# Kernel optimization log

Hardware: AMD Instinct MI355X
Metric: run time of the kernel (lower is better)

Reference implementation:

```python
import jax, jax.numpy as jnp
import numpy as np

B, S, E = 16, 1024, 512
D = 2 * E            # dim of concatenated embeddings, input to QKV and MLP
H1, H2 = 2048, 1024  # hidden_dims
SCALE = float(1.0 / np.sqrt(E))  # code scales by embedding_dim**0.5 (the init arg, not D)


def setup_inputs() -> dict:
    key = jax.random.key(0)
    k = jax.random.split(key, 12)

    def lin_w(kk, fan_in, fan_out):
        return jax.random.normal(kk, (fan_in, fan_out), jnp.float32) * float(1.0 / np.sqrt(fan_in))

    return {
        "emb1": jax.random.normal(k[0], (B, S, E), jnp.float32),
        "emb2": jax.random.normal(k[1], (B, S, E), jnp.float32),
        # query-row masks; all ones (a 0 would -inf an entire softmax row -> NaN)
        "mask1": jnp.ones((B, S // 2), jnp.int32),
        "mask2": jnp.ones((B, S // 2), jnp.int32),
        "Wq": lin_w(k[2], D, D), "bq": jnp.zeros((D,), jnp.float32),
        "Wk": lin_w(k[3], D, D), "bk": jnp.zeros((D,), jnp.float32),
        "Wv": lin_w(k[4], D, D), "bv": jnp.zeros((D,), jnp.float32),
        "W1": lin_w(k[5], D, H1), "b1": jnp.zeros((H1,), jnp.float32),
        "W2": lin_w(k[6], H1, H2), "b2": jnp.zeros((H2,), jnp.float32),
        "W3": lin_w(k[7], H2, 1), "b3": jnp.zeros((1,), jnp.float32),
    }


def reference(emb1, emb2, mask1, mask2, Wq, bq, Wk, bk, Wv, bv, W1, b1, W2, b2, W3, b3):
    x = jnp.concatenate([emb1, emb2], axis=-1)        # [B, S, D]
    mask = jnp.concatenate([mask1, mask2], axis=-1)   # [B, S] (query-row mask)

    # QKV self-attention with query-only mask
    Q = x @ Wq + bq
    K = x @ Wk + bk
    V = x @ Wv + bv
    scores = jnp.einsum("bqd,bkd->bqk", Q, K) * SCALE  # [B, S, S]
    scores = jnp.where(mask[:, :, None] == 0, -jnp.inf, scores)
    attn = jax.nn.softmax(scores, axis=-1)
    attended = jnp.einsum("bqk,bkd->bqd", attn, V)     # [B, S, D]

    # MLP head (Dropout is identity in eval mode)
    h = jax.nn.relu(attended @ W1 + b1)
    h = jax.nn.relu(h @ W2 + b2)
    logits = h @ W3 + b3                               # [B, S, 1]
    return jax.nn.sigmoid(logits)
```

## Files before the change

kernel.cpp:

```cpp
#include <hip/hip_runtime.h>
#include <math.h>

#define DEV __device__ __forceinline__
#define SB0() __builtin_amdgcn_sched_barrier(0)

typedef unsigned short u16;
typedef unsigned int   u32;
typedef __bf16 bf16x8 __attribute__((ext_vector_type(8)));
typedef float  f32x4  __attribute__((ext_vector_type(4)));
typedef u16    u16x8  __attribute__((ext_vector_type(8)));
typedef u16    u16x4  __attribute__((ext_vector_type(4)));

DEV u16 f2b(float f) {
  u32 u = __builtin_bit_cast(u32, f);
  u = (u + 0x7FFFu + ((u >> 16) & 1u)) >> 16;
  return (u16)u;
}
DEV float b2f(u16 h) { u32 u = (u32)h << 16; return __builtin_bit_cast(float, u); }

DEV void gl_lds16(const u16* g, u16* l) {
  __builtin_amdgcn_global_load_lds((const __attribute__((address_space(1))) void*)g,
                                   (__attribute__((address_space(3))) void*)l, 16, 0, 0);
}

__global__ __launch_bounds__(256) void prep(
    const float* __restrict__ e1, const float* __restrict__ e2, u16* __restrict__ xb,
    const float* __restrict__ Wq, const float* __restrict__ Wk, const float* __restrict__ Wv,
    const float* __restrict__ W1, const float* __restrict__ W2,
    u16* __restrict__ WTQKV, u16* __restrict__ W1T, u16* __restrict__ W2T,
    const float* __restrict__ bq, const float* __restrict__ bk, float* __restrict__ bf) {
  __shared__ float tile[64][65];
  const int bid = blockIdx.x;
  if (bid < 8192) {
    const size_t idx = ((size_t)bid * 256 + threadIdx.x) * 8;
    const int d = (int)(idx & 1023);
    const size_t row = idx >> 10;
    const float* s = (d < 512) ? (e1 + row * 512 + d) : (e2 + row * 512 + (d - 512));
    f32x4 a = *(const f32x4*)s;
    f32x4 b = *(const f32x4*)(s + 4);
    u16x8 o;
    o[0]=f2b(a[0]); o[1]=f2b(a[1]); o[2]=f2b(a[2]); o[3]=f2b(a[3]);
    o[4]=f2b(b[0]); o[5]=f2b(b[1]); o[6]=f2b(b[2]); o[7]=f2b(b[3]);
    *(u16x8*)(xb + idx) = o;
    return;
  }
  if (bid >= 9984) {
    int i = (bid - 9984) * 256 + threadIdx.x;
    bf[i] = (i < 1024) ? bq[i] : bk[i - 1024];
    return;
  }
  const float* W; u16* WT; int ldi, ldo, bx, by;
  if (bid < 8448)      { W = Wq; WT = WTQKV;              ldi = 1024; ldo = 1024; int v = bid - 8192; bx = v & 15; by = v >> 4; }
  else if (bid < 8704) { W = Wk; WT = WTQKV + 1024*1024;  ldi = 1024; ldo = 1024; int v = bid - 8448; bx = v & 15; by = v >> 4; }
  else if (bid < 8960) { W = Wv; WT = WTQKV + 2048*1024;  ldi = 1024; ldo = 1024; int v = bid - 8704; bx = v & 15; by = v >> 4; }
  else if (bid < 9472) { W = W1; WT = W1T;                ldi = 2048; ldo = 1024; int v = bid - 8960; bx = v & 31; by = v >> 5; }
  else                 { W = W2; WT = W2T;                ldi = 1024; ldo = 2048; int v = bid - 9472; bx = v & 15; by = v >> 4; }
  const int tx = threadIdx.x & 63, ty = threadIdx.x >> 6;
  const int r0 = by * 64, c0 = bx * 64;
#pragma unroll
  for (int i = 0; i < 16; ++i)
    tile[ty + 4*i][tx] = W[(size_t)(r0 + ty + 4*i) * ldi + c0 + tx];
  __syncthreads();
#pragma unroll
  for (int i = 0; i < 16; ++i)
    WT[(size_t)(c0 + ty + 4*i) * ldo + r0 + tx] = f2b(tile[tx][ty + 4*i]);
}

template<int MODE>
__global__ __launch_bounds__(512, 2) void gemm256(
    const u16* __restrict__ A, int lda, long long sA,
    const u16* __restrict__ B, int ldb, long long sB,
    void* __restrict__ C, int ldc, long long sC,
    const float* __restrict__ bias, float scale, int K,
    const int* __restrict__ mk1, const int* __restrict__ mk2,
    float* __restrict__ rsw, const float* __restrict__ w3, float* __restrict__ lg) {
  __shared__ __align__(16) u16 lds[2][2][16384];

  const int t  = threadIdx.x;
  const int ln = t & 63, wv = t >> 6;

  int bx, by, bz;
  {
    const int gx = gridDim.x, gy = gridDim.y, gz = gridDim.z;
    const int nwg = gx * gy * gz;
    const int F = (blockIdx.z * gy + blockIdx.y) * gx + blockIdx.x;
    const int q = nwg >> 3;
    const int L = (F & 7) * q + (F >> 3);
    if (gz > 1) {
      const int pb = gx * gy;
      bz = L / pb; const int r = L - bz * pb;
      by = r / gx; bx = r - by * gx;
    } else {
      bz = 0;
      const int sh = ((gy & 7) == 0) ? 8 : 4;
      const int sw = gx * sh;
      const int sy = L / sw; const int r = L - sy * sw;
      bx = r / sh; by = sy * sh + (r - bx * sh);
    }
  }
  const int m0 = by * 256, n0 = bx * 256;
  A += (size_t)bz * (size_t)sA; B += (size_t)bz * (size_t)sB;

  const int gl = (ln & 7) ^ (ln >> 3);
  const u16* gAs = A + (size_t)(m0 + (t >> 3)) * lda + gl * 8;
  const u16* gBs = B + (size_t)(n0 + (t >> 3)) * ldb + gl * 8;

  const int l15 = ln & 15, lhi = ln >> 4;
  const int wm = (wv >> 2) * 128, wn = (wv & 3) * 64;
  const int colk0 = ((lhi ^ (l15 & 7)) << 3);
  const int colk1 = (((4 + lhi) ^ (l15 & 7)) << 3);
  const int rcA = (wv >> 2) * 8192 + l15 * 64;
  const int rcB = ((wv & 3) >> 1) * 8192 + (wv & 1) * 4096 + l15 * 64;

  f32x4 acc[8][4] = {};
  bf16x8 Af[4][2], Bf[4][2];
  const int KT = K >> 6, NIT = KT >> 1;

#define STG(T, OP, H, LD, GS)                                              \
  if ((T) < KT) {                                                          \
    const u16* _s = (GS) + (size_t)(H) * 128 * (size_t)(LD) + (size_t)(T) * 64; \
    u16* _d = &lds[(T) & 1][OP][(H) * 8192 + wv * 512];                    \
    gl_lds16(_s, _d); gl_lds16(_s + 64 * (size_t)(LD), _d + 4096);         \
  }
#define RDA(BUF, ILO) {                                                    \
  _Pragma("unroll") for (int ii = 0; ii < 4; ++ii) {                       \
    Af[ii][0] = *(const bf16x8*)&lds[BUF][0][rcA + ((ILO) + ii) * 1024 + colk0]; \
    Af[ii][1] = *(const bf16x8*)&lds[BUF][0][rcA + ((ILO) + ii) * 1024 + colk1]; } }
#define RDB(BUF, JLO) {                                                    \
  _Pragma("unroll") for (int jj = 0; jj < 2; ++jj) {                       \
    Bf[(JLO) + jj][0] = *(const bf16x8*)&lds[BUF][1][rcB + ((JLO) + jj) * 1024 + colk0]; \
    Bf[(JLO) + jj][1] = *(const bf16x8*)&lds[BUF][1][rcB + ((JLO) + jj) * 1024 + colk1]; } }
#define MM(ILO, JLO) {                                                     \
  _Pragma("unroll") for (int ii = 0; ii < 4; ++ii)                         \
  _Pragma("unroll") for (int jj = 0; jj < 2; ++jj) {                       \
    acc[(ILO)+ii][(JLO)+jj] = __builtin_amdgcn_mfma_f32_16x16x32_bf16(Af[ii][0], Bf[(JLO)+jj][0], acc[(ILO)+ii][(JLO)+jj], 0, 0, 0); \
    acc[(ILO)+ii][(JLO)+jj] = __builtin_amdgcn_mfma_f32_16x16x32_bf16(Af[ii][1], Bf[(JLO)+jj][1], acc[(ILO)+ii][(JLO)+jj], 0, 0, 0); } }
#define BAR() __builtin_amdgcn_s_barrier()
#define PRIO(x) __builtin_amdgcn_s_setprio(x)

  STG(0, 0, 0, lda, gAs); STG(0, 0, 1, lda, gAs);
  STG(0, 1, 0, ldb, gBs); STG(0, 1, 1, ldb, gBs);
  STG(1, 1, 0, ldb, gBs); STG(1, 1, 1, ldb, gBs);
  asm volatile("s_waitcnt vmcnt(4)" ::: "memory");
  SB0(); BAR();

  for (int it = 0; it < NIT; ++it) {
    const int T0 = it << 1, T1 = T0 + 1;
    RDB(0, 0); RDA(0, 0); STG(T1, 0, 0, lda, gAs);
    BAR();
    PRIO(1); MM(0, 0); PRIO(0); BAR();
    RDB(0, 2); STG(T1, 0, 1, lda, gAs);
    BAR();
    PRIO(1); MM(0, 2); PRIO(0); BAR();
    RDA(0, 4); STG(T0 + 2, 1, 0, ldb, gBs);
    BAR();
    PRIO(1); MM(4, 0); PRIO(0); BAR();
    STG(T0 + 2, 1, 1, ldb, gBs);
    BAR();
    PRIO(1); MM(4, 2); PRIO(0);
    if (T0 + 2 < KT) { asm volatile("s_waitcnt vmcnt(4)" ::: "memory"); }
    else             { asm volatile("s_waitcnt vmcnt(0)" ::: "memory"); }
    SB0(); BAR();
    RDB(1, 0); RDA(1, 0); STG(T0 + 2, 0, 0, lda, gAs);
    BAR();
    PRIO(1); MM(0, 0); PRIO(0); BAR();
    RDB(1, 2); STG(T0 + 2, 0, 1, lda, gAs);
    BAR();
    PRIO(1); MM(0, 2); PRIO(0); BAR();
    RDA(1, 4); STG(T0 + 3, 1, 0, ldb, gBs);
    BAR();
    PRIO(1); MM(4, 0); PRIO(0); BAR();
    STG(T0 + 3, 1, 1, ldb, gBs);
    BAR();
    PRIO(1); MM(4, 2); PRIO(0);
    if (T0 + 3 < KT) { asm volatile("s_waitcnt vmcnt(4)" ::: "memory"); }
    SB0(); BAR();
  }
#undef STG
#undef RDA
#undef RDB
#undef MM
#undef BAR
#undef PRIO

  const size_t cb = (size_t)bz * (size_t)sC;

  if (MODE == 5) {
    float w3v[4];
#pragma unroll
    for (int j = 0; j < 4; ++j) w3v[j] = w3[n0 + wn + j * 16 + l15];
#pragma unroll
    for (int i = 0; i < 8; ++i) {
      const int rg = m0 + wm + i * 16 + lhi * 4;
#pragma unroll
      for (int r = 0; r < 4; ++r) {
        float s = 0.f;
#pragma unroll
        for (int j = 0; j < 4; ++j) {
          float v = acc[i][j][r] + bias[n0 + wn + j * 16 + l15];
          v = fmaxf(v, 0.f);
          s += v * w3v[j];
        }
        s += __shfl_xor(s, 1, 64); s += __shfl_xor(s, 2, 64);
        s += __shfl_xor(s, 4, 64); s += __shfl_xor(s, 8, 64);
        if (l15 == 0) atomicAdd(&lg[rg + r], s);
      }
    }
    return;
  }

  u16* ep = ((u16*)lds) + wv * 8192;

  if (MODE == 3) {
#pragma unroll
    for (int i = 0; i < 8; ++i) {
#pragma unroll
      for (int r = 0; r < 4; ++r) {
        const int rr = m0 + wm + i * 16 + lhi * 4 + r;
        const int mk = (rr < 512) ? mk1[bz * 512 + rr] : mk2[bz * 512 + rr - 512];
        const int lrow = i * 16 + lhi * 4 + r;
        float s = 0.f;
#pragma unroll
        for (int j = 0; j < 4; ++j) {
          float e = (mk != 0) ? __expf(acc[i][j][r] * scale) : 0.f;
          const u16 eb = f2b(e);
          s += b2f(eb);
          const int lcol = (j * 16 + l15) ^ (((lrow >> 2) & 7) << 3);
          ep[lrow * 64 + lcol] = eb;
        }
        s += __shfl_xor(s, 1, 64); s += __shfl_xor(s, 2, 64);
        s += __shfl_xor(s, 4, 64); s += __shfl_xor(s, 8, 64);
        if (l15 == 0) atomicAdd(&rsw[(size_t)bz * 1024 + rr], s);
      }
    }
  } else {
#pragma unroll
    for (int i = 0; i < 8; ++i) {
      const int rl = wm + i * 16 + lhi * 4;
      float rv[4];
#pragma unroll
      for (int r = 0; r < 4; ++r) {
        if (MODE == 2)      rv[r] = bias[m0 + rl + r];
        else if (MODE == 4) rv[r] = 1.f / rsw[(size_t)bz * 1024 + m0 + rl + r];
        else                rv[r] = 0.f;
      }
#pragma unroll
      for (int j = 0; j < 4; ++j) {
        const float cbv = (MODE == 0 || MODE == 1) ? bias[n0 + wn + j * 16 + l15] : 0.f;
#pragma unroll
        for (int r = 0; r < 4; ++r) {
          float v;
          if (MODE == 4)      v = acc[i][j][r] * rv[r];
          else if (MODE == 2) v = acc[i][j][r] + rv[r];
          else                v = acc[i][j][r] + cbv;
          if (MODE == 1) v = fmaxf(v, 0.f);
          const int lrow = i * 16 + lhi * 4 + r;
          const int lcol = (j * 16 + l15) ^ (((lrow >> 2) & 7) << 3);
          ep[lrow * 64 + lcol] = f2b(v);
        }
      }
    }
  }
  asm volatile("s_waitcnt lgkmcnt(0)" ::: "memory");
  SB0();
  const int l3 = ln >> 3, c0 = (ln & 7) * 8;
#pragma unroll
  for (int rep = 0; rep < 16; ++rep) {
    const int lr = rep * 8 + l3;
    const int cs = c0 ^ (((lr >> 2) & 7) << 3);
    u16x8 v = *(const u16x8*)&ep[lr * 64 + cs];
    *(u16x8*)((u16*)C + cb + (size_t)(m0 + wm + lr) * ldc + n0 + wn + c0) = v;
  }
}

__global__ __launch_bounds__(256) void sigmoid_k(
    const float* __restrict__ lg, const float* __restrict__ b3, float* __restrict__ out) {
  const int i = blockIdx.x * 256 + threadIdx.x;
  out[i] = 1.f / (1.f + __expf(-(lg[i] + b3[0])));
}

extern "C" void kernel_launch(void* const* d_in, const int* in_sizes, int n_in,
                              void* d_out, int out_size, void* d_ws, size_t ws_size,
                              hipStream_t stream) {
  (void)in_sizes; (void)n_in; (void)out_size; (void)ws_size;
  const float* emb1 = (const float*)d_in[0];
  const float* emb2 = (const float*)d_in[1];
  const int*   mask1 = (const int*)d_in[2];
  const int*   mask2 = (const int*)d_in[3];
  const float* Wq = (const float*)d_in[4];  const float* bq = (const float*)d_in[5];
  const float* Wk = (const float*)d_in[6];  const float* bk = (const float*)d_in[7];
  const float* Wv = (const float*)d_in[8];  const float* bv = (const float*)d_in[9];
  const float* W1 = (const float*)d_in[10]; const float* b1 = (const float*)d_in[11];
  const float* W2 = (const float*)d_in[12]; const float* b2 = (const float*)d_in[13];
  const float* W3 = (const float*)d_in[14]; const float* b3 = (const float*)d_in[15];

  char* ws = (char*)d_ws;
  u16*  XB    = (u16*)(ws + 0);
  u16*  QK    = (u16*)(ws + 33554432);
  u16*  VT    = (u16*)(ws + 100663296);
  u16*  ATT   = (u16*)(ws + 134217728);
  u16*  WTQKV = (u16*)(ws + 167772160);
  u16*  W1T   = (u16*)(ws + 174063616);
  u16*  W2T   = (u16*)(ws + 178257920);
  float* BF_  = (float*)(ws + 182452224);
  float* RS   = (float*)(ws + 182460416);
  float* LG   = (float*)(ws + 182525952);
  u16*  E     = XB;
  u16*  H1    = QK;
  float* out  = (float*)d_out;

  const float SCALE = 0.04419417382415922f;

  hipMemsetAsync(RS, 0, 131072, stream);

  prep<<<9992, 256, 0, stream>>>(emb1, emb2, XB, Wq, Wk, Wv, W1, W2,
                                 WTQKV, W1T, W2T, bq, bk, BF_);

  gemm256<0><<<dim3(8, 64, 1), 512, 0, stream>>>(
      XB, 1024, 0, WTQKV, 1024, 0, QK, 2048, 0, BF_, 1.f, 1024,
      nullptr, nullptr, nullptr, nullptr, nullptr);
  gemm256<2><<<dim3(64, 4, 1), 512, 0, stream>>>(
      WTQKV + 2048 * 1024, 1024, 0, XB, 1024, 0, VT, 16384, 0, bv, 1.f, 1024,
      nullptr, nullptr, nullptr, nullptr, nullptr);
  gemm256<3><<<dim3(4, 4, 16), 512, 0, stream>>>(
      QK, 2048, 2097152LL, QK + 1024, 2048, 2097152LL,
      E, 1024, 1048576LL, nullptr, SCALE, 1024,
      mask1, mask2, RS, nullptr, nullptr);
  gemm256<4><<<dim3(4, 4, 16), 512, 0, stream>>>(
      E, 1024, 1048576LL, VT, 16384, 1024LL,
      ATT, 1024, 1048576LL, nullptr, 1.f, 1024,
      nullptr, nullptr, RS, nullptr, nullptr);
  gemm256<1><<<dim3(8, 64, 1), 512, 0, stream>>>(
      ATT, 1024, 0, W1T, 1024, 0, H1, 2048, 0, b1, 1.f, 1024,
      nullptr, nullptr, nullptr, nullptr, nullptr);
  gemm256<5><<<dim3(4, 64, 1), 512, 0, stream>>>(
      H1, 2048, 0, W2T, 2048, 0, nullptr, 1024, 0, b2, 1.f, 2048,
      nullptr, nullptr, nullptr, W3, LG);
  sigmoid_k<<<64, 256, 0, stream>>>(LG, b3, out);
}
```

Before: 348.6 us.

## Shrink GEMM tile to 128x256 with BK=32 simple double-buffered loop

Replaces the 256x256, BK=64 GEMM with its hand-scheduled split-phase pipeline by a 128x256 tile using BK=32 K-steps and a simple double-buffered loop. Each step issues one A and two B global-to-LDS loads, reads 4+4 fragments and runs 16 MFMAs per wave. Smaller LDS use and fewer accumulators allow launch bounds of 4 blocks per SM, and grid sizes double to match. The goal is more occupancy and latency hiding, at the cost of half the reuse per tile, more LDS traffic per FLOP, and a full vmcnt(0) wait plus barrier every K-step.

```diff
diff --git a/kernel.cpp b/kernel.cpp
--- a/kernel.cpp
+++ b/kernel.cpp
@@ -9,7 +9,6 @@
 typedef __bf16 bf16x8 __attribute__((ext_vector_type(8)));
 typedef float  f32x4  __attribute__((ext_vector_type(4)));
 typedef u16    u16x8  __attribute__((ext_vector_type(8)));
-typedef u16    u16x4  __attribute__((ext_vector_type(4)));
 
 DEV u16 f2b(float f) {
   u32 u = __builtin_bit_cast(u32, f);
@@ -67,14 +66,14 @@
 }
 
 template<int MODE>
-__global__ __launch_bounds__(512, 2) void gemm256(
+__global__ __launch_bounds__(512, 4) void gemm256(
     const u16* __restrict__ A, int lda, long long sA,
     const u16* __restrict__ B, int ldb, long long sB,
     void* __restrict__ C, int ldc, long long sC,
     const float* __restrict__ bias, float scale, int K,
     const int* __restrict__ mk1, const int* __restrict__ mk2,
     float* __restrict__ rsw, const float* __restrict__ w3, float* __restrict__ lg) {
-  __shared__ __align__(16) u16 lds[2][2][16384];
+  __shared__ __align__(16) u16 lds[32768];
 
   const int t  = threadIdx.x;
   const int ln = t & 63, wv = t >> 6;
@@ -92,96 +91,79 @@
       by = r / gx; bx = r - by * gx;
     } else {
       bz = 0;
-      const int sh = ((gy & 7) == 0) ? 8 : 4;
-      const int sw = gx * sh;
+      const int sw = gx * 8;
       const int sy = L / sw; const int r = L - sy * sw;
-      bx = r / sh; by = sy * sh + (r - bx * sh);
+      bx = r >> 3; by = sy * 8 + (r & 7);
     }
   }
-  const int m0 = by * 256, n0 = bx * 256;
+  const int m0 = by * 128, n0 = bx * 256;
   A += (size_t)bz * (size_t)sA; B += (size_t)bz * (size_t)sB;
 
-  const int gl = (ln & 7) ^ (ln >> 3);
-  const u16* gAs = A + (size_t)(m0 + (t >> 3)) * lda + gl * 8;
-  const u16* gBs = B + (size_t)(n0 + (t >> 3)) * ldb + gl * 8;
+  const int srow = t >> 2;
+  const int sg   = (t & 3) ^ ((t >> 3) & 3);
+  const u16* gA = A + (size_t)(m0 + srow) * lda + sg * 8;
+  const u16* gB = B + (size_t)(n0 + srow) * ldb + sg * 8;
+  const size_t b128r = (size_t)128 * ldb;
+  const int ldst = wv * 512;
 
   const int l15 = ln & 15, lhi = ln >> 4;
-  const int wm = (wv >> 2) * 128, wn = (wv & 3) * 64;
-  const int colk0 = ((lhi ^ (l15 & 7)) << 3);
-  const int colk1 = (((4 + lhi) ^ (l15 & 7)) << 3);
-  const int rcA = (wv >> 2) * 8192 + l15 * 64;
-  const int rcB = ((wv & 3) >> 1) * 8192 + (wv & 1) * 4096 + l15 * 64;
-
-  f32x4 acc[8][4] = {};
-  bf16x8 Af[4][2], Bf[4][2];
-  const int KT = K >> 6, NIT = KT >> 1;
-
-#define STG(T, OP, H, LD, GS)                                              \
-  if ((T) < KT) {                                                          \
-    const u16* _s = (GS) + (size_t)(H) * 128 * (size_t)(LD) + (size_t)(T) * 64; \
-    u16* _d = &lds[(T) & 1][OP][(H) * 8192 + wv * 512];                    \
-    gl_lds16(_s, _d); gl_lds16(_s + 64 * (size_t)(LD), _d + 4096);         \
-  }
-#define RDA(BUF, ILO) {                                                    \
-  _Pragma("unroll") for (int ii = 0; ii < 4; ++ii) {                       \
-    Af[ii][0] = *(const bf16x8*)&lds[BUF][0][rcA + ((ILO) + ii) * 1024 + colk0]; \
-    Af[ii][1] = *(const bf16x8*)&lds[BUF][0][rcA + ((ILO) + ii) * 1024 + colk1]; } }
-#define RDB(BUF, JLO) {                                                    \
-  _Pragma("unroll") for (int jj = 0; jj < 2; ++jj) {                       \
-    Bf[(JLO) + jj][0] = *(const bf16x8*)&lds[BUF][1][rcB + ((JLO) + jj) * 1024 + colk0]; \
-    Bf[(JLO) + jj][1] = *(const bf16x8*)&lds[BUF][1][rcB + ((JLO) + jj) * 1024 + colk1]; } }
-#define MM(ILO, JLO) {                                                     \
-  _Pragma("unroll") for (int ii = 0; ii < 4; ++ii)                         \
-  _Pragma("unroll") for (int jj = 0; jj < 2; ++jj) {                       \
-    acc[(ILO)+ii][(JLO)+jj] = __builtin_amdgcn_mfma_f32_16x16x32_bf16(Af[ii][0], Bf[(JLO)+jj][0], acc[(ILO)+ii][(JLO)+jj], 0, 0, 0); \
-    acc[(ILO)+ii][(JLO)+jj] = __builtin_amdgcn_mfma_f32_16x16x32_bf16(Af[ii][1], Bf[(JLO)+jj][1], acc[(ILO)+ii][(JLO)+jj], 0, 0, 0); } }
-#define BAR() __builtin_amdgcn_s_barrier()
-#define PRIO(x) __builtin_amdgcn_s_setprio(x)
-
-  STG(0, 0, 0, lda, gAs); STG(0, 0, 1, lda, gAs);
-  STG(0, 1, 0, ldb, gBs); STG(0, 1, 1, ldb, gBs);
-  STG(1, 1, 0, ldb, gBs); STG(1, 1, 1, ldb, gBs);
-  asm volatile("s_waitcnt vmcnt(4)" ::: "memory");
-  SB0(); BAR();
-
-  for (int it = 0; it < NIT; ++it) {
-    const int T0 = it << 1, T1 = T0 + 1;
-    RDB(0, 0); RDA(0, 0); STG(T1, 0, 0, lda, gAs);
-    BAR();
-    PRIO(1); MM(0, 0); PRIO(0); BAR();
-    RDB(0, 2); STG(T1, 0, 1, lda, gAs);
-    BAR();
-    PRIO(1); MM(0, 2); PRIO(0); BAR();
-    RDA(0, 4); STG(T0 + 2, 1, 0, ldb, gBs);
-    BAR();
-    PRIO(1); MM(4, 0); PRIO(0); BAR();
-    STG(T0 + 2, 1, 1, ldb, gBs);
-    BAR();
-    PRIO(1); MM(4, 2); PRIO(0);
-    if (T0 + 2 < KT) { asm volatile("s_waitcnt vmcnt(4)" ::: "memory"); }
-    else             { asm volatile("s_waitcnt vmcnt(0)" ::: "memory"); }
-    SB0(); BAR();
-    RDB(1, 0); RDA(1, 0); STG(T0 + 2, 0, 0, lda, gAs);
-    BAR();
-    PRIO(1); MM(0, 0); PRIO(0); BAR();
-    RDB(1, 2); STG(T0 + 2, 0, 1, lda, gAs);
-    BAR();
-    PRIO(1); MM(0, 2); PRIO(0); BAR();
-    RDA(1, 4); STG(T0 + 3, 1, 0, ldb, gBs);
-    BAR();
-    PRIO(1); MM(4, 0); PRIO(0); BAR();
-    STG(T0 + 3, 1, 1, ldb, gBs);
-    BAR();
-    PRIO(1); MM(4, 2); PRIO(0);
-    if (T0 + 3 < KT) { asm volatile("s_waitcnt vmcnt(4)" ::: "memory"); }
-    SB0(); BAR();
-  }
-#undef STG
-#undef RDA
-#undef RDB
-#undef MM
-#undef BAR
-#undef PRIO
+  const int wm = (wv >> 2) * 64, wn = (wv & 3) * 64;
+
+  int offA[4], offB[4];
+#pragma unroll
+  for (int i = 0; i < 4; ++i) {
+    const int r = wm + i * 16 + l15;
+    offA[i] = r * 32 + ((lhi ^ ((r >> 1) & 3)) << 3);
+  }
+#pragma unroll
+  for (int j = 0; j < 4; ++j) {
+    const int r = wn + j * 16 + l15;
+    offB[j] = 4096 + r * 32 + ((lhi ^ ((r >> 1) & 3)) << 3);
+  }
+
+  f32x4 acc[4][4] = {};
+  const int KT = K >> 5;
+
+#define STAGE(T)                                                          \
+  {                                                                       \
+    const int rb = (T) & 1;                                               \
+    const u16* _a = gA + (size_t)(T) * 32;                                \
+    const u16* _b = gB + (size_t)(T) * 32;                                \
+    gl_lds16(_a, &lds[rb * 12288 + ldst]);                                \
+    gl_lds16(_b, &lds[rb * 12288 + 4096 + ldst]);                         \
+    gl_lds16(_b + b128r, &lds[rb * 12288 + 8192 + ldst]);                 \
+  }
+#define MF(i, j, Av, Bv) \
+  acc[i][j] = __builtin_amdgcn_mfma_f32_16x16x32_bf16(Av, Bv, acc[i][j], 0, 0, 0)
+
+  STAGE(0);
+  asm volatile("s_waitcnt vmcnt(0)" ::: "memory");
+  SB0();
+  __builtin_amdgcn_s_barrier();
+
+  for (int kt = 0; kt < KT; ++kt) {
+    if (kt + 1 < KT) STAGE(kt + 1);
+    const u16* bb = &lds[(kt & 1) * 12288];
+    bf16x8 a0 = *(const bf16x8*)&bb[offA[0]];
+    bf16x8 a1 = *(const bf16x8*)&bb[offA[1]];
+    bf16x8 a2 = *(const bf16x8*)&bb[offA[2]];
+    bf16x8 a3 = *(const bf16x8*)&bb[offA[3]];
+    bf16x8 b0 = *(const bf16x8*)&bb[offB[0]];
+    bf16x8 b1 = *(const bf16x8*)&bb[offB[1]];
+    bf16x8 b2 = *(const bf16x8*)&bb[offB[2]];
+    bf16x8 b3 = *(const bf16x8*)&bb[offB[3]];
+    __builtin_amdgcn_s_setprio(1);
+    MF(0,0,a0,b0); MF(0,1,a0,b1); MF(0,2,a0,b2); MF(0,3,a0,b3);
+    MF(1,0,a1,b0); MF(1,1,a1,b1); MF(1,2,a1,b2); MF(1,3,a1,b3);
+    MF(2,0,a2,b0); MF(2,1,a2,b1); MF(2,2,a2,b2); MF(2,3,a2,b3);
+    MF(3,0,a3,b0); MF(3,1,a3,b1); MF(3,2,a3,b2); MF(3,3,a3,b3);
+    __builtin_amdgcn_s_setprio(0);
+    asm volatile("s_waitcnt vmcnt(0)" ::: "memory");
+    SB0();
+    __builtin_amdgcn_s_barrier();
+  }
+#undef STAGE
+#undef MF
 
   const size_t cb = (size_t)bz * (size_t)sC;
 
@@ -190,7 +172,7 @@
 #pragma unroll
     for (int j = 0; j < 4; ++j) w3v[j] = w3[n0 + wn + j * 16 + l15];
 #pragma unroll
-    for (int i = 0; i < 8; ++i) {
+    for (int i = 0; i < 4; ++i) {
       const int rg = m0 + wm + i * 16 + lhi * 4;
 #pragma unroll
       for (int r = 0; r < 4; ++r) {
@@ -209,11 +191,11 @@
     return;
   }
 
-  u16* ep = ((u16*)lds) + wv * 8192;
+  u16* ep = lds + wv * 4096;
 
   if (MODE == 3) {
 #pragma unroll
-    for (int i = 0; i < 8; ++i) {
+    for (int i = 0; i < 4; ++i) {
 #pragma unroll
       for (int r = 0; r < 4; ++r) {
         const int rr = m0 + wm + i * 16 + lhi * 4 + r;
@@ -235,7 +217,7 @@
     }
   } else {
 #pragma unroll
-    for (int i = 0; i < 8; ++i) {
+    for (int i = 0; i < 4; ++i) {
       const int rl = wm + i * 16 + lhi * 4;
       float rv[4];
 #pragma unroll
@@ -265,7 +247,7 @@
   SB0();
   const int l3 = ln >> 3, c0 = (ln & 7) * 8;
 #pragma unroll
-  for (int rep = 0; rep < 16; ++rep) {
+  for (int rep = 0; rep < 8; ++rep) {
     const int lr = rep * 8 + l3;
     const int cs = c0 ^ (((lr >> 2) & 7) << 3);
     u16x8 v = *(const u16x8*)&ep[lr * 64 + cs];
@@ -316,24 +298,24 @@
   prep<<<9992, 256, 0, stream>>>(emb1, emb2, XB, Wq, Wk, Wv, W1, W2,
                                  WTQKV, W1T, W2T, bq, bk, BF_);
 
-  gemm256<0><<<dim3(8, 64, 1), 512, 0, stream>>>(
+  gemm256<0><<<dim3(8, 128, 1), 512, 0, stream>>>(
       XB, 1024, 0, WTQKV, 1024, 0, QK, 2048, 0, BF_, 1.f, 1024,
       nullptr, nullptr, nullptr, nullptr, nullptr);
-  gemm256<2><<<dim3(64, 4, 1), 512, 0, stream>>>(
+  gemm256<2><<<dim3(64, 8, 1), 512, 0, stream>>>(
       WTQKV + 2048 * 1024, 1024, 0, XB, 1024, 0, VT, 16384, 0, bv, 1.f, 1024,
       nullptr, nullptr, nullptr, nullptr, nullptr);
-  gemm256<3><<<dim3(4, 4, 16), 512, 0, stream>>>(
+  gemm256<3><<<dim3(4, 8, 16), 512, 0, stream>>>(
       QK, 2048, 2097152LL, QK + 1024, 2048, 2097152LL,
       E, 1024, 1048576LL, nullptr, SCALE, 1024,
       mask1, mask2, RS, nullptr, nullptr);
-  gemm256<4><<<dim3(4, 4, 16), 512, 0, stream>>>(
+  gemm256<4><<<dim3(4, 8, 16), 512, 0, stream>>>(
       E, 1024, 1048576LL, VT, 16384, 1024LL,
       ATT, 1024, 1048576LL, nullptr, 1.f, 1024,
       nullptr, nullptr, RS, nullptr, nullptr);
-  gemm256<1><<<dim3(8, 64, 1), 512, 0, stream>>>(
+  gemm256<1><<<dim3(8, 128, 1), 512, 0, stream>>>(
       ATT, 1024, 0, W1T, 1024, 0, H1, 2048, 0, b1, 1.f, 1024,
       nullptr, nullptr, nullptr, nullptr, nullptr);
-  gemm256<5><<<dim3(4, 64, 1), 512, 0, stream>>>(
+  gemm256<5><<<dim3(4, 128, 1), 512, 0, stream>>>(
       H1, 2048, 0, W2T, 2048, 0, nullptr, 1024, 0, b2, 1.f, 2048,
       nullptr, nullptr, nullptr, W3, LG);
   sigmoid_k<<<64, 256, 0, stream>>>(LG, b3, out);
```

Result: slower. 357.5 us (+2.5%).

## Fold Q and K projections into a single Wq·Wkᵀ product with rank-1 bias terms

Applied to the files above, without the earlier changes.

Instead of computing Q and K separately, precomputes M = Wq Wkᵀ in bf16 and a per-row x·M product, then forms scores as (xM)xᵀ. The bias terms become per-row and per-column vectors added in the softmax epilogue. This roughly halves the projection GEMM work. In exchange it adds small extra kernels and changes rounding because M is quantized to bf16.

```diff
diff --git a/kernel.cpp b/kernel.cpp
--- a/kernel.cpp
+++ b/kernel.cpp
@@ -9,7 +9,6 @@
 typedef __bf16 bf16x8 __attribute__((ext_vector_type(8)));
 typedef float  f32x4  __attribute__((ext_vector_type(4)));
 typedef u16    u16x8  __attribute__((ext_vector_type(8)));
-typedef u16    u16x4  __attribute__((ext_vector_type(4)));
 
 DEV u16 f2b(float f) {
   u32 u = __builtin_bit_cast(u32, f);
@@ -27,8 +26,8 @@
     const float* __restrict__ e1, const float* __restrict__ e2, u16* __restrict__ xb,
     const float* __restrict__ Wq, const float* __restrict__ Wk, const float* __restrict__ Wv,
     const float* __restrict__ W1, const float* __restrict__ W2,
-    u16* __restrict__ WTQKV, u16* __restrict__ W1T, u16* __restrict__ W2T,
-    const float* __restrict__ bq, const float* __restrict__ bk, float* __restrict__ bf) {
+    u16* __restrict__ Wqb, u16* __restrict__ Wkb,
+    u16* __restrict__ WvT, u16* __restrict__ W1T, u16* __restrict__ W2T) {
   __shared__ float tile[64][65];
   const int bid = blockIdx.x;
   if (bid < 8192) {
@@ -44,17 +43,23 @@
     *(u16x8*)(xb + idx) = o;
     return;
   }
-  if (bid >= 9984) {
-    int i = (bid - 9984) * 256 + threadIdx.x;
-    bf[i] = (i < 1024) ? bq[i] : bk[i - 1024];
+  if (bid < 9216) {
+    const int base = (bid < 8704) ? 8192 : 8704;
+    const float* src = (bid < 8704) ? Wq : Wk;
+    u16* dst = (bid < 8704) ? Wqb : Wkb;
+    const int off = ((bid - base) * 256 + threadIdx.x) * 8;
+    f32x4 a = *(const f32x4*)(src + off);
+    f32x4 b = *(const f32x4*)(src + off + 4);
+    u16x8 o;
+    o[0]=f2b(a[0]); o[1]=f2b(a[1]); o[2]=f2b(a[2]); o[3]=f2b(a[3]);
+    o[4]=f2b(b[0]); o[5]=f2b(b[1]); o[6]=f2b(b[2]); o[7]=f2b(b[3]);
+    *(u16x8*)(dst + off) = o;
     return;
   }
   const float* W; u16* WT; int ldi, ldo, bx, by;
-  if (bid < 8448)      { W = Wq; WT = WTQKV;              ldi = 1024; ldo = 1024; int v = bid - 8192; bx = v & 15; by = v >> 4; }
-  else if (bid < 8704) { W = Wk; WT = WTQKV + 1024*1024;  ldi = 1024; ldo = 1024; int v = bid - 8448; bx = v & 15; by = v >> 4; }
-  else if (bid < 8960) { W = Wv; WT = WTQKV + 2048*1024;  ldi = 1024; ldo = 1024; int v = bid - 8704; bx = v & 15; by = v >> 4; }
-  else if (bid < 9472) { W = W1; WT = W1T;                ldi = 2048; ldo = 1024; int v = bid - 8960; bx = v & 31; by = v >> 5; }
-  else                 { W = W2; WT = W2T;                ldi = 1024; ldo = 2048; int v = bid - 9472; bx = v & 15; by = v >> 4; }
+  if (bid < 9472)      { W = Wv; WT = WvT; ldi = 1024; ldo = 1024; int v = bid - 9216; bx = v & 15; by = v >> 4; }
+  else if (bid < 9984) { W = W1; WT = W1T; ldi = 2048; ldo = 1024; int v = bid - 9472; bx = v & 31; by = v >> 5; }
+  else                 { W = W2; WT = W2T; ldi = 1024; ldo = 2048; int v = bid - 9984; bx = v & 15; by = v >> 4; }
   const int tx = threadIdx.x & 63, ty = threadIdx.x >> 6;
   const int r0 = by * 64, c0 = bx * 64;
 #pragma unroll
@@ -64,6 +69,62 @@
 #pragma unroll
   for (int i = 0; i < 16; ++i)
     WT[(size_t)(c0 + ty + 4*i) * ldo + r0 + tx] = f2b(tile[tx][ty + 4*i]);
+}
+
+__global__ __launch_bounds__(256) void bias_vecs(
+    const float* __restrict__ Wq, const float* __restrict__ Wk,
+    const float* __restrict__ bq, const float* __restrict__ bk,
+    float* __restrict__ vq, float* __restrict__ vk, float* __restrict__ cc) {
+  const int bid = blockIdx.x;
+  if (bid == 512) {
+    __shared__ float red[256];
+    float s = 0.f;
+    for (int i = threadIdx.x; i < 1024; i += 256) s += bq[i] * bk[i];
+    red[threadIdx.x] = s; __syncthreads();
+    for (int o = 128; o > 0; o >>= 1) {
+      if ((int)threadIdx.x < o) red[threadIdx.x] += red[threadIdx.x + o];
+      __syncthreads();
+    }
+    if (threadIdx.x == 0) cc[0] = red[0];
+    return;
+  }
+  const float* W = (bid < 256) ? Wq : Wk;
+  const float* b = (bid < 256) ? bk : bq;
+  float* v = (bid < 256) ? vq : vk;
+  const int row = ((bid & 255) << 2) + (threadIdx.x >> 6);
+  const int ln = threadIdx.x & 63;
+  const float* p = W + (size_t)row * 1024 + ln * 16;
+  float s = 0.f;
+#pragma unroll
+  for (int m = 0; m < 16; ++m) s += p[m] * b[ln * 16 + m];
+#pragma unroll
+  for (int o = 32; o > 0; o >>= 1) s += __shfl_xor(s, o, 64);
+  if (ln == 0) v[row] = s;
+}
+
+__global__ __launch_bounds__(256) void uw_vecs(
+    const u16* __restrict__ xb, const float* __restrict__ vq,
+    const float* __restrict__ vk, const float* __restrict__ cc,
+    float* __restrict__ U, float* __restrict__ W_) {
+  const int row = blockIdx.x * 4 + (threadIdx.x >> 6);
+  const int ln = threadIdx.x & 63;
+  const u16* p = xb + (size_t)row * 1024 + ln * 16;
+  u16x8 x0 = *(const u16x8*)p;
+  u16x8 x1 = *(const u16x8*)(p + 8);
+  float dq = 0.f, dk = 0.f;
+#pragma unroll
+  for (int m = 0; m < 8; ++m) {
+    float xv = b2f(x0[m]);
+    dq += xv * vq[ln * 16 + m]; dk += xv * vk[ln * 16 + m];
+  }
+#pragma unroll
+  for (int m = 0; m < 8; ++m) {
+    float xv = b2f(x1[m]);
+    dq += xv * vq[ln * 16 + 8 + m]; dk += xv * vk[ln * 16 + 8 + m];
+  }
+#pragma unroll
+  for (int o = 32; o > 0; o >>= 1) { dq += __shfl_xor(dq, o, 64); dk += __shfl_xor(dk, o, 64); }
+  if (ln == 0) { U[row] = dq + cc[0]; W_[row] = dk; }
 }
 
 template<int MODE>
@@ -73,7 +134,9 @@
     void* __restrict__ C, int ldc, long long sC,
     const float* __restrict__ bias, float scale, int K,
     const int* __restrict__ mk1, const int* __restrict__ mk2,
-    float* __restrict__ rsw, const float* __restrict__ w3, float* __restrict__ lg) {
+    float* __restrict__ rsw, const float* __restrict__ uvec,
+    const float* __restrict__ wvec, const float* __restrict__ w3,
+    float* __restrict__ lg) {
   __shared__ __align__(16) u16 lds[2][2][16384];
 
   const int t  = threadIdx.x;
@@ -212,17 +275,22 @@
   u16* ep = ((u16*)lds) + wv * 8192;
 
   if (MODE == 3) {
+    float wv4[4];
+#pragma unroll
+    for (int j = 0; j < 4; ++j)
+      wv4[j] = wvec[(size_t)bz * 1024 + n0 + wn + j * 16 + l15];
 #pragma unroll
     for (int i = 0; i < 8; ++i) {
 #pragma unroll
       for (int r = 0; r < 4; ++r) {
         const int rr = m0 + wm + i * 16 + lhi * 4 + r;
         const int mk = (rr < 512) ? mk1[bz * 512 + rr] : mk2[bz * 512 + rr - 512];
+        const float uq = uvec[(size_t)bz * 1024 + rr];
         const int lrow = i * 16 + lhi * 4 + r;
         float s = 0.f;
 #pragma unroll
         for (int j = 0; j < 4; ++j) {
-          float e = (mk != 0) ? __expf(acc[i][j][r] * scale) : 0.f;
+          float e = (mk != 0) ? __expf((acc[i][j][r] + uq + wv4[j]) * scale) : 0.f;
           const u16 eb = f2b(e);
           s += b2f(eb);
           const int lcol = (j * 16 + l15) ^ (((lrow >> 2) & 7) << 3);
@@ -246,7 +314,7 @@
       }
 #pragma unroll
       for (int j = 0; j < 4; ++j) {
-        const float cbv = (MODE == 0 || MODE == 1) ? bias[n0 + wn + j * 16 + l15] : 0.f;
+        const float cbv = ((MODE == 0 || MODE == 1) && bias) ? bias[n0 + wn + j * 16 + l15] : 0.f;
 #pragma unroll
         for (int r = 0; r < 4; ++r) {
           float v;
@@ -296,45 +364,57 @@
 
   char* ws = (char*)d_ws;
   u16*  XB    = (u16*)(ws + 0);
-  u16*  QK    = (u16*)(ws + 33554432);
-  u16*  VT    = (u16*)(ws + 100663296);
+  u16*  XM    = (u16*)(ws + 33554432);
+  u16*  VT    = (u16*)(ws + 67108864);
+  u16*  E     = (u16*)(ws + 100663296);
   u16*  ATT   = (u16*)(ws + 134217728);
-  u16*  WTQKV = (u16*)(ws + 167772160);
-  u16*  W1T   = (u16*)(ws + 174063616);
-  u16*  W2T   = (u16*)(ws + 178257920);
-  float* BF_  = (float*)(ws + 182452224);
-  float* RS   = (float*)(ws + 182460416);
-  float* LG   = (float*)(ws + 182525952);
-  u16*  E     = XB;
-  u16*  H1    = QK;
+  u16*  WvT   = (u16*)(ws + 167772160);
+  u16*  Wqb   = (u16*)(ws + 169869312);
+  u16*  Wkb   = (u16*)(ws + 171966464);
+  u16*  MTb   = (u16*)(ws + 174063616);
+  u16*  W1T   = (u16*)(ws + 176160768);
+  u16*  W2T   = (u16*)(ws + 180355072);
+  float* VQ   = (float*)(ws + 184549376);
+  float* VK   = (float*)(ws + 184553472);
+  float* CC   = (float*)(ws + 184557568);
+  float* U    = (float*)(ws + 184561664);
+  float* W_   = (float*)(ws + 184627200);
+  float* RS   = (float*)(ws + 184692736);
+  float* LG   = (float*)(ws + 184758272);
+  u16*  H1    = XB;
   float* out  = (float*)d_out;
 
   const float SCALE = 0.04419417382415922f;
 
   hipMemsetAsync(RS, 0, 131072, stream);
 
-  prep<<<9992, 256, 0, stream>>>(emb1, emb2, XB, Wq, Wk, Wv, W1, W2,
-                                 WTQKV, W1T, W2T, bq, bk, BF_);
-
-  gemm256<0><<<dim3(8, 64, 1), 512, 0, stream>>>(
-      XB, 1024, 0, WTQKV, 1024, 0, QK, 2048, 0, BF_, 1.f, 1024,
-      nullptr, nullptr, nullptr, nullptr, nullptr);
+  prep<<<10496, 256, 0, stream>>>(emb1, emb2, XB, Wq, Wk, Wv, W1, W2,
+                                  Wqb, Wkb, WvT, W1T, W2T);
+  bias_vecs<<<513, 256, 0, stream>>>(Wq, Wk, bq, bk, VQ, VK, CC);
+  uw_vecs<<<4096, 256, 0, stream>>>(XB, VQ, VK, CC, U, W_);
+
+  gemm256<0><<<dim3(4, 4, 1), 512, 0, stream>>>(
+      Wkb, 1024, 0, Wqb, 1024, 0, MTb, 1024, 0, nullptr, 1.f, 1024,
+      nullptr, nullptr, nullptr, nullptr, nullptr, nullptr, nullptr);
+  gemm256<0><<<dim3(4, 64, 1), 512, 0, stream>>>(
+      XB, 1024, 0, MTb, 1024, 0, XM, 1024, 0, nullptr, 1.f, 1024,
+      nullptr, nullptr, nullptr, nullptr, nullptr, nullptr, nullptr);
   gemm256<2><<<dim3(64, 4, 1), 512, 0, stream>>>(
-      WTQKV + 2048 * 1024, 1024, 0, XB, 1024, 0, VT, 16384, 0, bv, 1.f, 1024,
-      nullptr, nullptr, nullptr, nullptr, nullptr);
+      WvT, 1024, 0, XB, 1024, 0, VT, 16384, 0, bv, 1.f, 1024,
+      nullptr, nullptr, nullptr, nullptr, nullptr, nullptr, nullptr);
   gemm256<3><<<dim3(4, 4, 16), 512, 0, stream>>>(
-      QK, 2048, 2097152LL, QK + 1024, 2048, 2097152LL,
+      XM, 1024, 1048576LL, XB, 1024, 1048576LL,
       E, 1024, 1048576LL, nullptr, SCALE, 1024,
-      mask1, mask2, RS, nullptr, nullptr);
+      mask1, mask2, RS, U, W_, nullptr, nullptr);
   gemm256<4><<<dim3(4, 4, 16), 512, 0, stream>>>(
       E, 1024, 1048576LL, VT, 16384, 1024LL,
       ATT, 1024, 1048576LL, nullptr, 1.f, 1024,
-      nullptr, nullptr, RS, nullptr, nullptr);
+      nullptr, nullptr, RS, nullptr, nullptr, nullptr, nullptr);
   gemm256<1><<<dim3(8, 64, 1), 512, 0, stream>>>(
       ATT, 1024, 0, W1T, 1024, 0, H1, 2048, 0, b1, 1.f, 1024,
-      nullptr, nullptr, nullptr, nullptr, nullptr);
+      nullptr, nullptr, nullptr, nullptr, nullptr, nullptr, nullptr);
   gemm256<5><<<dim3(4, 64, 1), 512, 0, stream>>>(
       H1, 2048, 0, W2T, 2048, 0, nullptr, 1024, 0, b2, 1.f, 2048,
-      nullptr, nullptr, nullptr, W3, LG);
+      nullptr, nullptr, nullptr, nullptr, nullptr, W3, LG);
   sigmoid_k<<<64, 256, 0, stream>>>(LG, b3, out);
 }
```

Result: slower. 368.0 us (+5.6%).

## Add 128x256-tile GEMM kernel with triple-buffered LDS for QK and W1 projections

Applied to the files above, without the earlier changes.

Introduces a new gemm128 kernel that uses 128x256 output tiles, a 3-stage LDS ring filled by direct global-to-LDS loads, and launch bounds allowing four workgroups per CU. It is used for the QK projection and the first MLP layer, doubling the grid to 1024 workgroups. The aim is better CU occupancy, more latency hiding and better load balance across the MI355X's compute units. In exchange each tile reuses its operands less, so global and LDS traffic per FLOP rises.

```diff
diff --git a/kernel.cpp b/kernel.cpp
--- a/kernel.cpp
+++ b/kernel.cpp
@@ -9,7 +9,6 @@
 typedef __bf16 bf16x8 __attribute__((ext_vector_type(8)));
 typedef float  f32x4  __attribute__((ext_vector_type(4)));
 typedef u16    u16x8  __attribute__((ext_vector_type(8)));
-typedef u16    u16x4  __attribute__((ext_vector_type(4)));
 
 DEV u16 f2b(float f) {
   u32 u = __builtin_bit_cast(u32, f);
@@ -273,6 +272,129 @@
   }
 }
 
+template<int MODE>
+__global__ __launch_bounds__(512, 4) void gemm128(
+    const u16* __restrict__ A, int lda,
+    const u16* __restrict__ B, int ldb,
+    void* __restrict__ C, int ldc,
+    const float* __restrict__ bias, int K) {
+  __shared__ __align__(16) u16 lds[3 * 12288];
+
+  const int t  = threadIdx.x;
+  const int ln = t & 63, wv = t >> 6;
+
+  int bx, by;
+  {
+    const int gx = gridDim.x, gy = gridDim.y;
+    const int nwg = gx * gy;
+    const int F = blockIdx.y * gx + blockIdx.x;
+    const int q = nwg >> 3;
+    const int L = (F & 7) * q + (F >> 3);
+    const int sw = gx * 8;
+    const int sy = L / sw; const int r = L - sy * sw;
+    bx = r >> 3; by = sy * 8 + (r & 7);
+  }
+  const int m0 = by * 128, n0 = bx * 256;
+
+  const int srow = t >> 2;
+  const int sg   = (t & 3) ^ ((t >> 3) & 3);
+  const u16* gA = A + (size_t)(m0 + srow) * lda + sg * 8;
+  const u16* gB = B + (size_t)(n0 + srow) * ldb + sg * 8;
+  const size_t b128r = (size_t)128 * ldb;
+  const int ldst = wv * 512;
+
+  const int l15 = ln & 15, lhi = ln >> 4;
+  const int wm = (wv >> 2) * 64, wn = (wv & 3) * 64;
+
+  int offA[4], offB[4];
+#pragma unroll
+  for (int i = 0; i < 4; ++i) {
+    const int r = wm + i * 16 + l15;
+    offA[i] = r * 32 + ((lhi ^ ((r >> 1) & 3)) << 3);
+  }
+#pragma unroll
+  for (int j = 0; j < 4; ++j) {
+    const int r = wn + j * 16 + l15;
+    offB[j] = 4096 + r * 32 + ((lhi ^ ((r >> 1) & 3)) << 3);
+  }
+
+  f32x4 acc[4][4] = {};
+  const int KT = K >> 5;
+
+#define STAGE(T, RB)                                                      \
+  {                                                                       \
+    const u16* _a = gA + (size_t)(T) * 32;                                \
+    const u16* _b = gB + (size_t)(T) * 32;                                \
+    gl_lds16(_a, &lds[(RB) * 12288 + ldst]);                              \
+    gl_lds16(_b, &lds[(RB) * 12288 + 4096 + ldst]);                       \
+    gl_lds16(_b + b128r, &lds[(RB) * 12288 + 8192 + ldst]);               \
+  }
+#define MF(i, j, Av, Bv) \
+  acc[i][j] = __builtin_amdgcn_mfma_f32_16x16x32_bf16(Av, Bv, acc[i][j], 0, 0, 0)
+
+  STAGE(0, 0); STAGE(1, 1);
+  asm volatile("s_waitcnt vmcnt(3)" ::: "memory");
+  SB0();
+  __builtin_amdgcn_s_barrier();
+
+  int rb_read = 0, rb_stage = 2;
+  for (int kt = 0; kt < KT; ++kt) {
+    if (kt + 2 < KT) STAGE(kt + 2, rb_stage);
+    const u16* bb = &lds[rb_read * 12288];
+    bf16x8 a0 = *(const bf16x8*)&bb[offA[0]];
+    bf16x8 a1 = *(const bf16x8*)&bb[offA[1]];
+    bf16x8 a2 = *(const bf16x8*)&bb[offA[2]];
+    bf16x8 a3 = *(const bf16x8*)&bb[offA[3]];
+    bf16x8 b0 = *(const bf16x8*)&bb[offB[0]];
+    bf16x8 b1 = *(const bf16x8*)&bb[offB[1]];
+    bf16x8 b2 = *(const bf16x8*)&bb[offB[2]];
+    bf16x8 b3 = *(const bf16x8*)&bb[offB[3]];
+    __builtin_amdgcn_s_setprio(1);
+    MF(0,0,a0,b0); MF(0,1,a0,b1); MF(0,2,a0,b2); MF(0,3,a0,b3);
+    MF(1,0,a1,b0); MF(1,1,a1,b1); MF(1,2,a1,b2); MF(1,3,a1,b3);
+    MF(2,0,a2,b0); MF(2,1,a2,b1); MF(2,2,a2,b2); MF(2,3,a2,b3);
+    MF(3,0,a3,b0); MF(3,1,a3,b1); MF(3,2,a3,b2); MF(3,3,a3,b3);
+    __builtin_amdgcn_s_setprio(0);
+    if (kt < KT - 2)       { asm volatile("s_waitcnt vmcnt(3)" ::: "memory"); }
+    else if (kt == KT - 2) { asm volatile("s_waitcnt vmcnt(0)" ::: "memory"); }
+    if (kt < KT - 1) {
+      SB0();
+      __builtin_amdgcn_s_barrier();
+    }
+    rb_read  = (rb_read  == 2) ? 0 : rb_read + 1;
+    rb_stage = (rb_stage == 2) ? 0 : rb_stage + 1;
+  }
+#undef STAGE
+#undef MF
+
+  u16* ep = lds + wv * 4096;
+#pragma unroll
+  for (int i = 0; i < 4; ++i) {
+#pragma unroll
+    for (int j = 0; j < 4; ++j) {
+      const float cbv = bias[n0 + wn + j * 16 + l15];
+#pragma unroll
+      for (int r = 0; r < 4; ++r) {
+        float v = acc[i][j][r] + cbv;
+        if (MODE == 1) v = fmaxf(v, 0.f);
+        const int lrow = i * 16 + lhi * 4 + r;
+        const int lcol = (j * 16 + l15) ^ (((lrow >> 2) & 7) << 3);
+        ep[lrow * 64 + lcol] = f2b(v);
+      }
+    }
+  }
+  asm volatile("s_waitcnt lgkmcnt(0)" ::: "memory");
+  SB0();
+  const int l3 = ln >> 3, c0 = (ln & 7) * 8;
+#pragma unroll
+  for (int rep = 0; rep < 8; ++rep) {
+    const int lr = rep * 8 + l3;
+    const int cs = c0 ^ (((lr >> 2) & 7) << 3);
+    u16x8 v = *(const u16x8*)&ep[lr * 64 + cs];
+    *(u16x8*)((u16*)C + (size_t)(m0 + wm + lr) * ldc + n0 + wn + c0) = v;
+  }
+}
+
 __global__ __launch_bounds__(256) void sigmoid_k(
     const float* __restrict__ lg, const float* __restrict__ b3, float* __restrict__ out) {
   const int i = blockIdx.x * 256 + threadIdx.x;
@@ -316,9 +438,8 @@
   prep<<<9992, 256, 0, stream>>>(emb1, emb2, XB, Wq, Wk, Wv, W1, W2,
                                  WTQKV, W1T, W2T, bq, bk, BF_);
 
-  gemm256<0><<<dim3(8, 64, 1), 512, 0, stream>>>(
-      XB, 1024, 0, WTQKV, 1024, 0, QK, 2048, 0, BF_, 1.f, 1024,
-      nullptr, nullptr, nullptr, nullptr, nullptr);
+  gemm128<0><<<dim3(8, 128, 1), 512, 0, stream>>>(
+      XB, 1024, WTQKV, 1024, QK, 2048, BF_, 1024);
   gemm256<2><<<dim3(64, 4, 1), 512, 0, stream>>>(
       WTQKV + 2048 * 1024, 1024, 0, XB, 1024, 0, VT, 16384, 0, bv, 1.f, 1024,
       nullptr, nullptr, nullptr, nullptr, nullptr);
@@ -330,9 +451,8 @@
       E, 1024, 1048576LL, VT, 16384, 1024LL,
       ATT, 1024, 1048576LL, nullptr, 1.f, 1024,
       nullptr, nullptr, RS, nullptr, nullptr);
-  gemm256<1><<<dim3(8, 64, 1), 512, 0, stream>>>(
-      ATT, 1024, 0, W1T, 1024, 0, H1, 2048, 0, b1, 1.f, 1024,
-      nullptr, nullptr, nullptr, nullptr, nullptr);
+  gemm128<1><<<dim3(8, 128, 1), 512, 0, stream>>>(
+      ATT, 1024, W1T, 1024, H1, 2048, b1, 1024);
   gemm256<5><<<dim3(4, 64, 1), 512, 0, stream>>>(
       H1, 2048, 0, W2T, 2048, 0, nullptr, 1024, 0, b2, 1.f, 2048,
       nullptr, nullptr, nullptr, W3, LG);
```

Measured after the change: 354.3 us. No clear change (+1.6%).
